# Performance work log

Measured on AMD Instinct MI355X. Metric: run time of the kernel, lower is better.

## Reference

```python
import jax, jax.numpy as jnp
import numpy as np

NUM_HEADS = 16
TEMPERATURE = 1.0
LN_EPS = 1e-5


def _layer_norm(x, g, b):
    m = x.mean(-1, keepdims=True)
    v = ((x - m) ** 2).mean(-1, keepdims=True)
    return (x - m) / jnp.sqrt(v + LN_EPS) * g + b


def _forward(input_ids, k, tok_emb, pos_emb, Wqkv, bqkv, Wo, bo, ln1g, ln1b, ln2g, ln2b,
             W1, b1, W2, b2, Wr, br, We1, be1, We2, be2, Wout, bout):
    B, S = input_ids.shape
    D = tok_emb.shape[1]
    L = Wqkv.shape[0]
    H = NUM_HEADS
    dh = D // H
    # embeddings: token + learned position
    x = tok_emb[input_ids] + pos_emb[:S][None, :, :]  # [B,S,D]

    # post-norm TransformerEncoder (PyTorch default), gelu FFN, no mask (attention_mask=None path)
    for i in range(L):
        qkv = jnp.einsum('bsd,ed->bse', x, Wqkv[i]) + bqkv[i]        # [B,S,3D]
        q, kk, v = jnp.split(qkv, 3, axis=-1)
        to_heads = lambda t: t.reshape(B, S, H, dh).transpose(0, 2, 1, 3)  # [B,H,S,dh]
        q, kk, v = to_heads(q), to_heads(kk), to_heads(v)
        scores = jnp.einsum('bhqd,bhkd->bhqk', q, kk) / np.float32(np.sqrt(dh))
        attn = jax.nn.softmax(scores, axis=-1)
        ctx = jnp.einsum('bhqk,bhkd->bhqd', attn, v).transpose(0, 2, 1, 3).reshape(B, S, D)
        attn_out = jnp.einsum('bsd,ed->bse', ctx, Wo[i]) + bo[i]
        x = _layer_norm(x + attn_out, ln1g[i], ln1b[i])
        ff = jnp.einsum('bsf,df->bsd',
                        jax.nn.gelu(jnp.einsum('bsd,fd->bsf', x, W1[i]) + b1[i], approximate=False),
                        W2[i]) + b2[i]
        x = _layer_norm(x + ff, ln2g[i], ln2b[i])

    # router: top-k over softmax(logits / T), renormalized top-k weights
    T = B * S
    h = x.reshape(T, D)
    rlogits = h @ Wr.T + br                         # [T,E]
    probs = jax.nn.softmax(rlogits / TEMPERATURE, axis=-1)
    w, idx = jax.lax.top_k(probs, k)                # [T,k]
    w = w / w.sum(-1, keepdims=True)

    # experts (GELU MLP), computed densely and combined with one-hot routing weights
    E = We1.shape[0]
    hid = jax.nn.gelu(jnp.einsum('td,efd->etf', h, We1) + be1[:, None, :], approximate=False)  # [E,T,F]
    eout = jnp.einsum('etf,edf->etd', hid, We2) + be2[:, None, :]                              # [E,T,D]
    comb = (jax.nn.one_hot(idx, E, dtype=h.dtype) * w[..., None]).sum(1)                       # [T,E]
    moe = jnp.einsum('etd,te->td', eout, comb)                                                 # [T,D]

    logits = moe @ Wout.T + bout
    return logits.reshape(B, S, -1)


def setup_inputs() -> dict:
    key = jax.random.key(0)
    ks = iter(jax.random.split(key, 32))
    B, S, D, L, V, E, F, K = 4, 512, 1024, 12, 32000, 8, 4096, 2
    p = lambda shape: jax.random.normal(next(ks), shape, dtype=jnp.float32) * 0.02
    return {
        'input_ids': jax.random.randint(next(ks), (B, S), 0, V, dtype=jnp.int32),
        'k': K,
        'tok_emb': p((V, D)), 'pos_emb': p((1024, D)),
        'Wqkv': p((L, 3 * D, D)), 'bqkv': jnp.zeros((L, 3 * D), jnp.float32),
        'Wo': p((L, D, D)), 'bo': jnp.zeros((L, D), jnp.float32),
        'ln1g': jnp.ones((L, D), jnp.float32), 'ln1b': jnp.zeros((L, D), jnp.float32),
        'ln2g': jnp.ones((L, D), jnp.float32), 'ln2b': jnp.zeros((L, D), jnp.float32),
        'W1': p((L, F, D)), 'b1': jnp.zeros((L, F), jnp.float32),
        'W2': p((L, D, F)), 'b2': jnp.zeros((L, D), jnp.float32),
        'Wr': p((E, D)), 'br': jnp.zeros((E,), jnp.float32),
        'We1': p((E, F, D)), 'be1': jnp.zeros((E, F), jnp.float32),
        'We2': p((E, D, F)), 'be2': jnp.zeros((E, D), jnp.float32),
        'Wout': p((V, D)), 'bout': jnp.zeros((V,), jnp.float32),
    }


def reference(input_ids, k, tok_emb, pos_emb, Wqkv, bqkv, Wo, bo, ln1g, ln1b, ln2g, ln2b,
              W1, b1, W2, b2, Wr, br, We1, be1, We2, be2, Wout, bout):
    return _forward(input_ids, k, tok_emb, pos_emb, Wqkv, bqkv, Wo, bo, ln1g, ln1b, ln2g, ln2b,
                    W1, b1, W2, b2, Wr, br, We1, be1, We2, be2, Wout, bout)
```

## Files before the change

### kernel.cpp

```cpp
#include <hip/hip_runtime.h>
#include <cstdint>
#include <cstddef>

#define DI __device__ __forceinline__

typedef __attribute__((ext_vector_type(8))) short short8;
typedef __attribute__((ext_vector_type(4))) float f32x4;
typedef unsigned short u16;

DI u16 f2bf(float f) {
  union { float f; unsigned u; } v; v.f = f;
  unsigned r = v.u + 0x7fffu + ((v.u >> 16) & 1u);
  return (u16)(r >> 16);
}
DI float bf2f(u16 h) {
  union { unsigned u; float f; } v; v.u = ((unsigned)h) << 16;
  return v.f;
}

DI void gload_lds16(const void* g, void* l) {
  __builtin_amdgcn_global_load_lds(
      (const __attribute__((address_space(1))) void*)g,
      (__attribute__((address_space(3))) void*)l, 16, 0, 0);
}

DI void atomAddF(float* p, float v) {
  __hip_atomic_fetch_add(p, v, __ATOMIC_RELAXED, __HIP_MEMORY_SCOPE_AGENT);
}

DI void split4(float4 v, uint2& hi, uint2& lo) {
  unsigned u0 = __float_as_uint(v.x), u1 = __float_as_uint(v.y);
  unsigned u2 = __float_as_uint(v.z), u3 = __float_as_uint(v.w);
  unsigned r0 = (u0 + 0x7fffu + ((u0 >> 16) & 1u)) & 0xffff0000u;
  unsigned r1 = (u1 + 0x7fffu + ((u1 >> 16) & 1u)) & 0xffff0000u;
  unsigned r2 = (u2 + 0x7fffu + ((u2 >> 16) & 1u)) & 0xffff0000u;
  unsigned r3 = (u3 + 0x7fffu + ((u3 >> 16) & 1u)) & 0xffff0000u;
  unsigned l0 = __float_as_uint(v.x - __uint_as_float(r0));
  unsigned l1 = __float_as_uint(v.y - __uint_as_float(r1));
  unsigned l2 = __float_as_uint(v.z - __uint_as_float(r2));
  unsigned l3 = __float_as_uint(v.w - __uint_as_float(r3));
  hi.x = __builtin_amdgcn_perm(r1, r0, 0x07060302u);
  hi.y = __builtin_amdgcn_perm(r3, r2, 0x07060302u);
  lo.x = __builtin_amdgcn_perm(l1, l0, 0x07060302u);
  lo.y = __builtin_amdgcn_perm(l3, l2, 0x07060302u);
}

template<int BM, int BN, int WGM, int WGN, int OUTMODE, bool GELU, int GATHER,
         bool BF32, int SPLITK, int TERMS>
__global__ __launch_bounds__(256)
void gemm_bt(const u16* __restrict__ A, int lda, long planeA, long offA_hi, long offA_lo,
             const void* __restrict__ Bv, int ldb, long planeB, long offB_hi, long offB_lo,
             void* __restrict__ Cv, int ldc, long planeC, long offC_hi, long offC_lo,
             int K, float alpha,
             const float* __restrict__ bias, long offBias,
             const float* __restrict__ wf,
             const int* __restrict__ glist,
             const int* __restrict__ gcnt,
             const int* __restrict__ gmap,
             const int* __restrict__ gaoff)
{
  constexpr int BK = 32;
  constexpr int WM = BM / WGM, WN = BN / WGN;
  constexpr int FM = WM / 16, FN = WN / 16;
  constexpr int A_INST = (BM * BK) / (256 * 8);
  constexpr int B_INST = (BN * BK) / (256 * 8);
  constexpr int BF_INST = (BN * BK) / (256 * 4);
  static_assert(A_INST * 2048 == BM * BK && B_INST * 2048 == BN * BK, "tile sizing");

  int bx = blockIdx.x, by = blockIdx.y;
  {
    const int gy = gridDim.y;
    const int nwg = gridDim.x * gy;
    const int id = bx * gy + by;
    const int q = nwg >> 3, r = nwg & 7;
    const int xcd = id & 7, pos = id >> 3;
    const int nid = ((xcd < r) ? xcd * (q + 1) : r * (q + 1) + (xcd - r) * q) + pos;
    bx = nid / gy; by = nid % gy;
  }

  int e = 0, sk = 0, zb = 0, zh = 0, cnte = 0, lsb = 0;
  if constexpr (GATHER != 0) {
    e = gmap[by];
    if (e < 0) return;
    cnte = gcnt[e];
    lsb = by * BM - gaoff[e];
    if constexpr (SPLITK > 1) sk = blockIdx.z;
  } else if constexpr (SPLITK > 1) {
    sk = blockIdx.z;
  } else {
    zb = blockIdx.z >> 4; zh = blockIdx.z & 15;
  }

  __shared__ __align__(16) u16 Ash[BM * BK];
  __shared__ __align__(16) u16 Asl[BM * BK];
  __shared__ __align__(16) u16 Bsh[BN * BK];
  __shared__ __align__(16) u16 Bsl[(TERMS == 3) ? BN * BK : 8];

  const int tid = threadIdx.x;
  const int lane = tid & 63, wid = tid >> 6;

  const u16* Ab = A + (size_t)zb * offA_hi + (size_t)zh * offA_lo
                    + (GATHER == 1 ? 0 : (size_t)(by * BM) * lda);
  const u16* Bb = (const u16*)Bv + (size_t)zb * offB_hi + (size_t)zh * offB_lo
                    + (size_t)(bx * BN) * ldb;
  const float* Bfb = (const float*)Bv + (size_t)e * offB_hi
                    + (size_t)(bx * BN) * ldb;

  int grow[A_INST];
  if constexpr (GATHER == 1) {
#pragma unroll
    for (int j = 0; j < A_INST; ++j) {
      int ee = (j * 256 + tid) * 8;
      int sl = lsb + (ee >> 5);
      grow[j] = (sl < cnte) ? (glist[e * 2048 + sl] >> 1) : 0;
    }
  }

  const int wm0 = (wid / WGN) * WM;
  const int wn0 = (wid % WGN) * WN;
  const int fr = lane & 15;
  const int kb = (lane >> 4) * 8;

  f32x4 acc[FM][FN] = {};

  const int Ksp = K / SPLITK;
  const int kbeg = sk * Ksp, kend = kbeg + Ksp;
  for (int k0 = kbeg; k0 < kend; k0 += BK) {
    __syncthreads();
#pragma unroll
    for (int j = 0; j < A_INST; ++j) {
      int ee = (j * 256 + tid) * 8;
      size_t gs = (GATHER == 1 ? (size_t)grow[j] : (size_t)(ee >> 5)) * lda + k0 + (ee & 31);
      gload_lds16(Ab + gs,          (char*)Ash + (size_t)ee * 2);
      gload_lds16(Ab + planeA + gs, (char*)Asl + (size_t)ee * 2);
    }
    if constexpr (BF32) {
#pragma unroll
      for (int j = 0; j < BF_INST; ++j) {
        int ee = (j * 256 + tid) * 4;
        float4 v = *(const float4*)(Bfb + (size_t)(ee >> 5) * ldb + k0 + (ee & 31));
        uint2 hi, lo;
        split4(v, hi, lo);
        *(uint2*)&Bsh[ee] = hi;
        if constexpr (TERMS == 3) *(uint2*)&Bsl[ee] = lo;
      }
    } else {
#pragma unroll
      for (int j = 0; j < B_INST; ++j) {
        int ee = (j * 256 + tid) * 8;
        size_t gs = (size_t)(ee >> 5) * ldb + k0 + (ee & 31);
        gload_lds16(Bb + gs, (char*)Bsh + (size_t)ee * 2);
        if constexpr (TERMS == 3)
          gload_lds16(Bb + planeB + gs, (char*)Bsl + (size_t)ee * 2);
      }
    }
    __syncthreads();

    short8 ah[FM], al_[FM], bh[FN], bl[FN];
#pragma unroll
    for (int mi = 0; mi < FM; ++mi) {
      int off = (wm0 + mi * 16 + fr) * BK + kb;
      ah[mi]  = *(const short8*)&Ash[off];
      al_[mi] = *(const short8*)&Asl[off];
    }
#pragma unroll
    for (int ni = 0; ni < FN; ++ni) {
      int off = (wn0 + ni * 16 + fr) * BK + kb;
      bh[ni] = *(const short8*)&Bsh[off];
      if constexpr (TERMS == 3) bl[ni] = *(const short8*)&Bsl[off];
    }
#pragma unroll
    for (int mi = 0; mi < FM; ++mi)
#pragma unroll
      for (int ni = 0; ni < FN; ++ni) {
        acc[mi][ni] = __builtin_amdgcn_mfma_f32_16x16x32_bf16(ah[mi],  bh[ni], acc[mi][ni], 0, 0, 0);
        if constexpr (TERMS == 3)
          acc[mi][ni] = __builtin_amdgcn_mfma_f32_16x16x32_bf16(ah[mi], bl[ni], acc[mi][ni], 0, 0, 0);
        acc[mi][ni] = __builtin_amdgcn_mfma_f32_16x16x32_bf16(al_[mi], bh[ni], acc[mi][ni], 0, 0, 0);
      }
  }
  __syncthreads();

  const size_t offC = (size_t)zb * offC_hi + (size_t)zh * offC_lo;
  const int row0 = by * BM + wm0 + (lane >> 4) * 4;
  const int col0 = bx * BN + wn0 + fr;
  const float* biasp = bias ? bias + (size_t)e * offBias : nullptr;
  const bool addBias = biasp && (SPLITK == 1 || sk == 0);

#pragma unroll
  for (int mi = 0; mi < FM; ++mi) {
#pragma unroll
    for (int ni = 0; ni < FN; ++ni) {
      const int col = col0 + ni * 16;
      const float bv = addBias ? biasp[col] : 0.f;
#pragma unroll
      for (int r = 0; r < 4; ++r) {
        const int row = row0 + mi * 16 + r;
        float v = acc[mi][ni][r] * alpha + bv;
        if constexpr (GELU) v = 0.5f * v * (1.f + erff(v * 0.70710678118f));
        if constexpr (OUTMODE == 4) {
          int sl = row - gaoff[e];
          if (sl < cnte) {
            int lv = glist[e * 2048 + sl];
            int tok = lv >> 1, rank = lv & 1;
            float* p = (float*)Cv + (size_t)rank * planeC + (size_t)tok * ldc + col;
            float out = wf[tok * 2 + rank] * v;
            if constexpr (SPLITK > 1) atomAddF(p, out); else *p = out;
          }
        } else {
          const size_t idx = offC + (size_t)row * ldc + col;
          if constexpr (OUTMODE == 1) {
            u16 h = f2bf(v);
            u16 l = f2bf(v - bf2f(h));
            ((u16*)Cv)[idx] = h;
            ((u16*)Cv)[idx + planeC] = l;
          } else if constexpr (OUTMODE == 3) {
            if constexpr (SPLITK > 1) atomAddF((float*)Cv + idx, v);
            else ((float*)Cv)[idx] += v;
          } else {
            ((float*)Cv)[idx] = v;
          }
        }
      }
    }
  }
}

__global__ __launch_bounds__(512)
void attn_scores(const u16* __restrict__ qkv, long planeQ,
                 u16* __restrict__ probs, long planeP)
{
  constexpr int BK = 32, S = 512;
  extern __shared__ __align__(16) char smem[];
  u16* Ash = (u16*)smem;
  u16* Asl = Ash + 128 * 32;
  u16* Bsh = Asl + 128 * 32;
  u16* Bsl = Bsh + 512 * 32;
  float* redM = (float*)(Bsl + 512 * 32);
  float* redS = redM + 512;

  const int tid = threadIdx.x, lane = tid & 63, wid = tid >> 6;
  const int bh = blockIdx.z, zb = bh >> 4, zh = bh & 15;
  const int qt = blockIdx.y;
  const u16* Ab = qkv + (size_t)zb * (512 * 3072) + (size_t)zh * 64
                      + (size_t)(qt * 128) * 3072;
  const u16* Bb = qkv + (size_t)zb * (512 * 3072) + (size_t)zh * 64 + 1024;

  const int wr = wid >> 2, wc = wid & 3;
  const int fr = lane & 15, kb = (lane >> 4) * 8, g = lane >> 4;

  f32x4 acc[4][8] = {};

  for (int k0 = 0; k0 < 64; k0 += BK) {
    __syncthreads();
    {
      int ee = tid * 8;
      size_t gs = (size_t)(ee >> 5) * 3072 + k0 + (ee & 31);
      gload_lds16(Ab + gs,          (char*)Ash + (size_t)ee * 2);
      gload_lds16(Ab + planeQ + gs, (char*)Asl + (size_t)ee * 2);
    }
#pragma unroll
    for (int j = 0; j < 4; ++j) {
      int ee = (j * 512 + tid) * 8;
      size_t gs = (size_t)(ee >> 5) * 3072 + k0 + (ee & 31);
      gload_lds16(Bb + gs,          (char*)Bsh + (size_t)ee * 2);
      gload_lds16(Bb + planeQ + gs, (char*)Bsl + (size_t)ee * 2);
    }
    __syncthreads();

    short8 ah[4], al_[4];
#pragma unroll
    for (int mi = 0; mi < 4; ++mi) {
      int off = (wr * 64 + mi * 16 + fr) * BK + kb;
      ah[mi]  = *(const short8*)&Ash[off];
      al_[mi] = *(const short8*)&Asl[off];
    }
#pragma unroll
    for (int ni = 0; ni < 8; ++ni) {
      int off = (wc * 128 + ni * 16 + fr) * BK + kb;
      short8 bhv = *(const short8*)&Bsh[off];
      short8 blv = *(const short8*)&Bsl[off];
#pragma unroll
      for (int mi = 0; mi < 4; ++mi) {
        acc[mi][ni] = __builtin_amdgcn_mfma_f32_16x16x32_bf16(ah[mi],  bhv, acc[mi][ni], 0, 0, 0);
        acc[mi][ni] = __builtin_amdgcn_mfma_f32_16x16x32_bf16(ah[mi],  blv, acc[mi][ni], 0, 0, 0);
        acc[mi][ni] = __builtin_amdgcn_mfma_f32_16x16x32_bf16(al_[mi], bhv, acc[mi][ni], 0, 0, 0);
      }
    }
  }

#pragma unroll
  for (int mi = 0; mi < 4; ++mi)
#pragma unroll
    for (int ni = 0; ni < 8; ++ni)
#pragma unroll
      for (int r = 0; r < 4; ++r) acc[mi][ni][r] *= 0.125f;

  float m[4][4];
#pragma unroll
  for (int mi = 0; mi < 4; ++mi)
#pragma unroll
    for (int r = 0; r < 4; ++r) {
      float v = acc[mi][0][r];
#pragma unroll
      for (int ni = 1; ni < 8; ++ni) v = fmaxf(v, acc[mi][ni][r]);
      v = fmaxf(v, __shfl_xor(v, 1));
      v = fmaxf(v, __shfl_xor(v, 2));
      v = fmaxf(v, __shfl_xor(v, 4));
      v = fmaxf(v, __shfl_xor(v, 8));
      m[mi][r] = v;
    }
  if (fr == 0) {
#pragma unroll
    for (int mi = 0; mi < 4; ++mi)
#pragma unroll
      for (int r = 0; r < 4; ++r)
        redM[wr * 256 + (g * 4 + mi * 16 + r) * 4 + wc] = m[mi][r];
  }
  __syncthreads();
#pragma unroll
  for (int mi = 0; mi < 4; ++mi)
#pragma unroll
    for (int r = 0; r < 4; ++r) {
      const float* p = &redM[wr * 256 + (g * 4 + mi * 16 + r) * 4];
      m[mi][r] = fmaxf(fmaxf(p[0], p[1]), fmaxf(p[2], p[3]));
    }

  float ssum[4][4];
#pragma unroll
  for (int mi = 0; mi < 4; ++mi)
#pragma unroll
    for (int r = 0; r < 4; ++r) {
      float ss = 0.f;
#pragma unroll
      for (int ni = 0; ni < 8; ++ni) {
        float p = __expf(acc[mi][ni][r] - m[mi][r]);
        acc[mi][ni][r] = p;
        ss += p;
      }
      ss += __shfl_xor(ss, 1);
      ss += __shfl_xor(ss, 2);
      ss += __shfl_xor(ss, 4);
      ss += __shfl_xor(ss, 8);
      ssum[mi][r] = ss;
    }
  if (fr == 0) {
#pragma unroll
    for (int mi = 0; mi < 4; ++mi)
#pragma unroll
      for (int r = 0; r < 4; ++r)
        redS[wr * 256 + (g * 4 + mi * 16 + r) * 4 + wc] = ssum[mi][r];
  }
  __syncthreads();

  const size_t base = (size_t)bh * S * S + (size_t)(qt * 128 + wr * 64) * S;
#pragma unroll
  for (int mi = 0; mi < 4; ++mi)
#pragma unroll
    for (int r = 0; r < 4; ++r) {
      const float* p = &redS[wr * 256 + (g * 4 + mi * 16 + r) * 4];
      const float inv = 1.f / (p[0] + p[1] + p[2] + p[3]);
      const size_t rowoff = base + (size_t)(g * 4 + mi * 16 + r) * S;
#pragma unroll
      for (int ni = 0; ni < 8; ++ni) {
        float pv = acc[mi][ni][r] * inv;
        u16 h = f2bf(pv);
        u16 l = f2bf(pv - bf2f(h));
        size_t idx = rowoff + wc * 128 + ni * 16 + fr;
        probs[idx] = h;
        probs[idx + planeP] = l;
      }
    }
}

__global__ __launch_bounds__(256)
void embed_kernel(const int* __restrict__ ids, const float* __restrict__ tok,
                  const float* __restrict__ pos, float* __restrict__ x,
                  u16* __restrict__ xs, long plane)
{
  const int t = blockIdx.x, c = threadIdx.x;
  const int id = ids[t], s = t & 511;
  float4 tv = ((const float4*)(tok + (size_t)id * 1024))[c];
  float4 pv = ((const float4*)(pos + (size_t)s * 1024))[c];
  float o[4] = {tv.x + pv.x, tv.y + pv.y, tv.z + pv.z, tv.w + pv.w};
  ((float4*)(x + (size_t)t * 1024))[c] = *(float4*)o;
  uint2 uh, ul;
  u16 h0 = f2bf(o[0]), h1 = f2bf(o[1]), h2 = f2bf(o[2]), h3 = f2bf(o[3]);
  uh.x = (unsigned)h0 | ((unsigned)h1 << 16);
  uh.y = (unsigned)h2 | ((unsigned)h3 << 16);
  ul.x = (unsigned)f2bf(o[0] - bf2f(h0)) | ((unsigned)f2bf(o[1] - bf2f(h1)) << 16);
  ul.y = (unsigned)f2bf(o[2] - bf2f(h2)) | ((unsigned)f2bf(o[3] - bf2f(h3)) << 16);
  const size_t idx = (size_t)t * 1024 + c * 4;
  *(uint2*)(xs + idx) = uh;
  *(uint2*)(xs + plane + idx) = ul;
}

__global__ __launch_bounds__(256)
void ln_kernel(float* __restrict__ x, const float* __restrict__ g,
               const float* __restrict__ b, u16* __restrict__ xs, long plane)
{
  const int row = blockIdx.x, t = threadIdx.x;
  float4 xv = ((const float4*)(x + (size_t)row * 1024))[t];
  float s = xv.x + xv.y + xv.z + xv.w;
  float q = xv.x * xv.x + xv.y * xv.y + xv.z * xv.z + xv.w * xv.w;
#pragma unroll
  for (int o = 32; o; o >>= 1) { s += __shfl_xor(s, o); q += __shfl_xor(q, o); }
  __shared__ float ss[4], qq[4];
  const int wid = t >> 6;
  if ((t & 63) == 0) { ss[wid] = s; qq[wid] = q; }
  __syncthreads();
  s = ss[0] + ss[1] + ss[2] + ss[3];
  q = qq[0] + qq[1] + qq[2] + qq[3];
  const float mean = s * (1.f / 1024.f);
  const float var = q * (1.f / 1024.f) - mean * mean;
  const float rstd = 1.f / sqrtf(var + 1e-5f);
  float4 gv = ((const float4*)g)[t];
  float4 bv = ((const float4*)b)[t];
  float o[4];
  o[0] = (xv.x - mean) * rstd * gv.x + bv.x;
  o[1] = (xv.y - mean) * rstd * gv.y + bv.y;
  o[2] = (xv.z - mean) * rstd * gv.z + bv.z;
  o[3] = (xv.w - mean) * rstd * gv.w + bv.w;
  ((float4*)(x + (size_t)row * 1024))[t] = *(float4*)o;
  uint2 uh, ul;
  u16 h0 = f2bf(o[0]), h1 = f2bf(o[1]), h2 = f2bf(o[2]), h3 = f2bf(o[3]);
  uh.x = (unsigned)h0 | ((unsigned)h1 << 16);
  uh.y = (unsigned)h2 | ((unsigned)h3 << 16);
  ul.x = (unsigned)f2bf(o[0] - bf2f(h0)) | ((unsigned)f2bf(o[1] - bf2f(h1)) << 16);
  ul.y = (unsigned)f2bf(o[2] - bf2f(h2)) | ((unsigned)f2bf(o[3] - bf2f(h3)) << 16);
  const size_t idx = (size_t)row * 1024 + t * 4;
  *(uint2*)(xs + idx) = uh;
  *(uint2*)(xs + plane + idx) = ul;
}

__global__ __launch_bounds__(256)
void vtrans_kernel(const u16* __restrict__ qkv, u16* __restrict__ vT,
                   long planeQ, long planeV)
{
  __shared__ u16 tile[64][68];
  const u16* src = qkv + (size_t)blockIdx.z * planeQ;
  u16* dst = vT + (size_t)blockIdx.z * planeV;
  const int s0 = blockIdx.x << 6;
  const int bh = blockIdx.y, b = bh >> 4, h = bh & 15;
  const int t = threadIdx.x;
#pragma unroll
  for (int j = 0; j < 16; ++j) {
    int idx = j * 256 + t;
    int sl = idx >> 6, d = idx & 63;
    tile[sl][d] = src[(size_t)(b * 512 + s0 + sl) * 3072 + 2048 + h * 64 + d];
  }
  __syncthreads();
#pragma unroll
  for (int j = 0; j < 16; ++j) {
    int idx = j * 256 + t;
    int d = idx >> 6, sl = idx & 63;
    dst[(size_t)bh * (64 * 512) + (size_t)d * 512 + s0 + sl] = tile[sl][d];
  }
}

__global__ __launch_bounds__(256)
void router_kernel(const float* __restrict__ x, const float* __restrict__ Wr,
                   const float* __restrict__ br, int2* __restrict__ er,
                   float2* __restrict__ wf)
{
  const int lane = threadIdx.x & 63, wid = threadIdx.x >> 6;
  const int t = blockIdx.x * 4 + wid;
  const float* xr = x + (size_t)t * 1024;
  float xv[16];
#pragma unroll
  for (int j = 0; j < 16; ++j) xv[j] = xr[j * 64 + lane];
  float p[8];
#pragma unroll
  for (int e = 0; e < 8; ++e) {
    const float* wr = Wr + (size_t)e * 1024;
    float s = 0.f;
#pragma unroll
    for (int j = 0; j < 16; ++j) s += xv[j] * wr[j * 64 + lane];
#pragma unroll
    for (int o = 32; o; o >>= 1) s += __shfl_xor(s, o);
    p[e] = s + br[e];
  }
  float m = p[0];
#pragma unroll
  for (int e = 1; e < 8; ++e) m = fmaxf(m, p[e]);
#pragma unroll
  for (int e = 0; e < 8; ++e) p[e] = __expf(p[e] - m);
  int i1 = -1; float v1 = -1.f;
#pragma unroll
  for (int e = 0; e < 8; ++e) if (p[e] > v1) { v1 = p[e]; i1 = e; }
  int i2 = -1; float v2 = -1.f;
#pragma unroll
  for (int e = 0; e < 8; ++e) if (e != i1 && p[e] > v2) { v2 = p[e]; i2 = e; }
  const float inv = 1.f / (v1 + v2);
  if (lane == 0) {
    er[t] = make_int2(i1, i2);
    wf[t] = make_float2(v1 * inv, v2 * inv);
  }
}

__global__ __launch_bounds__(256)
void build_lists(const int2* __restrict__ er, int* __restrict__ cnt,
                 int* __restrict__ list)
{
  const int t = blockIdx.x * 256 + threadIdx.x;
  int2 e = er[t];
  int s0 = atomicAdd(&cnt[e.x], 1); list[e.x * 2048 + s0] = t * 2;
  int s1 = atomicAdd(&cnt[e.y], 1); list[e.y * 2048 + s1] = t * 2 + 1;
}

__global__ void finalize_lists(const int* __restrict__ cnt, int* __restrict__ aoff,
                               int* __restrict__ block2e, int nb)
{
  if (threadIdx.x != 0 || blockIdx.x != 0) return;
  for (int b = 0; b < nb; ++b) block2e[b] = -1;
  int off = 0;
  for (int e = 0; e < 8; ++e) {
    aoff[e] = off;
    int pe = ((cnt[e] + 127) >> 7) << 7;
    for (int b = off >> 7; b < (off + pe) >> 7; ++b) block2e[b] = e;
    off += pe;
  }
  aoff[8] = off;
}

__global__ __launch_bounds__(256)
void combine_split(const float* __restrict__ o0, const float* __restrict__ o1,
                   u16* __restrict__ dh, long plane)
{
  const long i = ((long)blockIdx.x * 256 + threadIdx.x) * 8;
  float4 a0 = ((const float4*)o0)[i / 4];
  float4 a1 = ((const float4*)o0)[i / 4 + 1];
  float4 b0 = ((const float4*)o1)[i / 4];
  float4 b1 = ((const float4*)o1)[i / 4 + 1];
  float v[8] = {a0.x + b0.x, a0.y + b0.y, a0.z + b0.z, a0.w + b0.w,
                a1.x + b1.x, a1.y + b1.y, a1.z + b1.z, a1.w + b1.w};
  u16 h[8], l[8];
#pragma unroll
  for (int j = 0; j < 8; ++j) {
    h[j] = f2bf(v[j]);
    l[j] = f2bf(v[j] - bf2f(h[j]));
  }
  uint4 uh, ul;
  uh.x = (unsigned)h[0] | ((unsigned)h[1] << 16); ul.x = (unsigned)l[0] | ((unsigned)l[1] << 16);
  uh.y = (unsigned)h[2] | ((unsigned)h[3] << 16); ul.y = (unsigned)l[2] | ((unsigned)l[3] << 16);
  uh.z = (unsigned)h[4] | ((unsigned)h[5] << 16); ul.z = (unsigned)l[4] | ((unsigned)l[5] << 16);
  uh.w = (unsigned)h[6] | ((unsigned)h[7] << 16); ul.w = (unsigned)l[6] | ((unsigned)l[7] << 16);
  ((uint4*)dh)[i / 8] = uh;
  ((uint4*)(dh + plane))[i / 8] = ul;
}


extern "C" void kernel_launch(void* const* d_in, const int* in_sizes, int n_in,
                              void* d_out, int out_size, void* d_ws, size_t ws_size,
                              hipStream_t stream)
{
  (void)in_sizes; (void)n_in; (void)out_size;
  const int*   ids  = (const int*)d_in[0];
  const float* tok  = (const float*)d_in[2];
  const float* pos  = (const float*)d_in[3];
  const float* Wqkv = (const float*)d_in[4];
  const float* bqkv = (const float*)d_in[5];
  const float* Wo   = (const float*)d_in[6];
  const float* bo   = (const float*)d_in[7];
  const float* ln1g = (const float*)d_in[8];
  const float* ln1b = (const float*)d_in[9];
  const float* ln2g = (const float*)d_in[10];
  const float* ln2b = (const float*)d_in[11];
  const float* W1   = (const float*)d_in[12];
  const float* b1   = (const float*)d_in[13];
  const float* W2   = (const float*)d_in[14];
  const float* b2   = (const float*)d_in[15];
  const float* Wr   = (const float*)d_in[16];
  const float* br   = (const float*)d_in[17];
  const float* We1  = (const float*)d_in[18];
  const float* be1  = (const float*)d_in[19];
  const float* We2  = (const float*)d_in[20];
  const float* be2  = (const float*)d_in[21];
  const float* Wout = (const float*)d_in[22];
  const float* bout = (const float*)d_in[23];

  constexpr int T = 2048, D = 1024, S = 512, Bb = 4, H = 16, dh = 64, F = 4096,
                L = 12, E = 8, V = 32000;
  constexpr int NB = (2 * T + E * 127) / 128 + 1;

  constexpr long PX  = (long)T * D;
  constexpr long PQ  = (long)T * 3 * D;
  constexpr long PFE = (long)(NB * 128) * F;
  constexpr long PV  = (long)Bb * H * dh * S;
  constexpr long PSC = (long)Bb * H * S * S;

  char* w = (char*)d_ws;
  size_t o = 0;
  auto alloc = [&](size_t bytes) -> void* {
    void* p = w + o; o = (o + bytes + 255) & ~(size_t)255; return p;
  };
  float* x    = (float*)alloc((size_t)T * D * 4);
  u16* xs   = (u16*)alloc((size_t)2 * PX * 2);
  u16* moes = (u16*)alloc((size_t)2 * PX * 2);
  u16* qkvs = (u16*)alloc((size_t)2 * PQ * 2);
  u16* ctxs = (u16*)alloc((size_t)2 * PX * 2);
  size_t bigsz = (size_t)2 * ((PSC > PFE ? PSC : PFE)) * 2;
  u16* big  = (u16*)alloc(bigsz);
  u16* ffs  = big;
  u16* scs  = big;
  u16* vTs  = (u16*)alloc((size_t)2 * PV * 2);
  float* outr = (float*)alloc((size_t)2 * PX * 4);
  int2*   er  = (int2*)alloc((size_t)T * 8);
  float2* wf  = (float2*)alloc((size_t)T * 8);
  int*    cnt = (int*)alloc((size_t)E * 4);
  int*    list= (int*)alloc((size_t)E * T * 4);
  int*    aoff= (int*)alloc((size_t)(E + 1) * 4);
  int*    b2e = (int*)alloc((size_t)NB * 4);
  if (o > ws_size) return;

  embed_kernel<<<T, 256, 0, stream>>>(ids, tok, pos, x, xs, PX);

  constexpr size_t ATTN_LDS = (4096 + 4096 + 16384 + 16384) * 2 + 2 * 512 * 4;

  for (int l = 0; l < L; ++l) {
    gemm_bt<128,128,2,2,1,false,0,true,1,3><<<dim3(3 * D / 128, T / 128, 1), 256, 0, stream>>>(
        xs, D, PX, 0, 0, Wqkv + (size_t)l * 3 * D * D, D, 0, 0, 0,
        qkvs, 3 * D, PQ, 0, 0, D, 1.f, bqkv + (size_t)l * 3 * D, 0,
        nullptr, nullptr, nullptr, nullptr, nullptr);
    vtrans_kernel<<<dim3(S / 64, Bb * H, 2), 256, 0, stream>>>(qkvs, vTs, PQ, PV);
    attn_scores<<<dim3(1, S / 128, Bb * H), 512, ATTN_LDS, stream>>>(qkvs, PQ, scs, PSC);
    gemm_bt<64,64,2,2,1,false,0,false,1,3><<<dim3(1, S / 64, Bb * H), 256, 0, stream>>>(
        scs, S, PSC, (long)H * S * S, (long)S * S,
        vTs, S, PV,  (long)H * dh * S, (long)dh * S,
        ctxs, D, PX, (long)S * D, (long)dh,
        S, 1.f, nullptr, 0, nullptr, nullptr, nullptr, nullptr, nullptr);
    gemm_bt<128,128,2,2,3,false,0,true,2,3><<<dim3(D / 128, T / 128, 2), 256, 0, stream>>>(
        ctxs, D, PX, 0, 0, Wo + (size_t)l * D * D, D, 0, 0, 0,
        x, D, 0, 0, 0, D, 1.f, bo + (size_t)l * D, 0,
        nullptr, nullptr, nullptr, nullptr, nullptr);
    ln_kernel<<<T, 256, 0, stream>>>(x, ln1g + (size_t)l * D, ln1b + (size_t)l * D, xs, PX);
    gemm_bt<128,128,2,2,1,true,0,true,1,3><<<dim3(F / 128, T / 128, 1), 256, 0, stream>>>(
        xs, D, PX, 0, 0, W1 + (size_t)l * F * D, D, 0, 0, 0,
        ffs, F, (long)T * F, 0, 0, D, 1.f, b1 + (size_t)l * F, 0,
        nullptr, nullptr, nullptr, nullptr, nullptr);
    gemm_bt<128,128,2,2,3,false,0,true,4,3><<<dim3(D / 128, T / 128, 4), 256, 0, stream>>>(
        ffs, F, (long)T * F, 0, 0, W2 + (size_t)l * D * F, F, 0, 0, 0,
        x, D, 0, 0, 0, F, 1.f, b2 + (size_t)l * D, 0,
        nullptr, nullptr, nullptr, nullptr, nullptr);
    ln_kernel<<<T, 256, 0, stream>>>(x, ln2g + (size_t)l * D, ln2b + (size_t)l * D, xs, PX);
  }

  router_kernel<<<T / 4, 256, 0, stream>>>(x, Wr, br, er, wf);
  hipMemsetAsync(cnt, 0, E * 4, stream);
  build_lists<<<T / 256, 256, 0, stream>>>(er, cnt, list);
  finalize_lists<<<1, 64, 0, stream>>>(cnt, aoff, b2e, NB);
  hipMemsetAsync(outr, 0, (size_t)2 * PX * 4, stream);

  gemm_bt<128,128,2,2,1,true,1,true,1,2><<<dim3(F / 128, NB, 1), 256, 0, stream>>>(
      xs, D, PX, 0, 0, We1, D, 0, (long)F * D, 0,
      ffs, F, PFE, 0, 0, D, 1.f, be1, F,
      nullptr, list, cnt, b2e, aoff);
  gemm_bt<128,128,2,2,4,false,2,true,2,2><<<dim3(D / 128, NB, 2), 256, 0, stream>>>(
      ffs, F, PFE, 0, 0, We2, F, 0, (long)D * F, 0,
      outr, D, PX, 0, 0, F, 1.f, be2, D,
      (const float*)wf, list, cnt, b2e, aoff);

  combine_split<<<(PX / 2048), 256, 0, stream>>>(outr, outr + PX, moes, PX);

  gemm_bt<128,128,2,2,0,false,0,true,1,2><<<dim3(V / 128, T / 128, 1), 256, 0, stream>>>(
      moes, D, PX, 0, 0, Wout, D, 0, 0, 0,
      (float*)d_out, V, 0, 0, 0,
      D, 1.f, bout, 0, nullptr, nullptr, nullptr, nullptr, nullptr);
}
```

Measured before the change: 4.619 ms.

## Fuse attention softmax with P·V and pre-convert output projection weights to bf16

```diff
diff --git a/kernel.cpp b/kernel.cpp
--- a/kernel.cpp
+++ b/kernel.cpp
@@ -227,8 +227,9 @@
 }
 
 __global__ __launch_bounds__(512)
-void attn_scores(const u16* __restrict__ qkv, long planeQ,
-                 u16* __restrict__ probs, long planeP)
+void attn_fused(const u16* __restrict__ qkv, long planeQ,
+                const u16* __restrict__ vT, long planeV,
+                u16* __restrict__ ctxs, long planeC)
 {
   constexpr int BK = 32, S = 512;
   extern __shared__ __align__(16) char smem[];
@@ -238,6 +239,10 @@
   u16* Bsl = Bsh + 512 * 32;
   float* redM = (float*)(Bsl + 512 * 32);
   float* redS = redM + 512;
+  u16* Ph = (u16*)smem;
+  u16* Pl = Ph + 128 * 32;
+  u16* Vh = Pl + 128 * 32;
+  u16* Vl = Vh + 64 * 32;
 
   const int tid = threadIdx.x, lane = tid & 63, wid = tid >> 6;
   const int bh = blockIdx.z, zb = bh >> 4, zh = bh & 15;
@@ -245,6 +250,7 @@
   const u16* Ab = qkv + (size_t)zb * (512 * 3072) + (size_t)zh * 64
                       + (size_t)(qt * 128) * 3072;
   const u16* Bb = qkv + (size_t)zb * (512 * 3072) + (size_t)zh * 64 + 1024;
+  const u16* vt = vT + (size_t)bh * (64 * 512);
 
   const int wr = wid >> 2, wc = wid & 3;
   const int fr = lane & 15, kb = (lane >> 4) * 8, g = lane >> 4;
@@ -353,23 +359,70 @@
   }
   __syncthreads();
 
-  const size_t base = (size_t)bh * S * S + (size_t)(qt * 128 + wr * 64) * S;
 #pragma unroll
   for (int mi = 0; mi < 4; ++mi)
 #pragma unroll
     for (int r = 0; r < 4; ++r) {
       const float* p = &redS[wr * 256 + (g * 4 + mi * 16 + r) * 4];
       const float inv = 1.f / (p[0] + p[1] + p[2] + p[3]);
-      const size_t rowoff = base + (size_t)(g * 4 + mi * 16 + r) * S;
-#pragma unroll
-      for (int ni = 0; ni < 8; ++ni) {
-        float pv = acc[mi][ni][r] * inv;
-        u16 h = f2bf(pv);
-        u16 l = f2bf(pv - bf2f(h));
-        size_t idx = rowoff + wc * 128 + ni * 16 + fr;
-        probs[idx] = h;
-        probs[idx + planeP] = l;
-      }
+#pragma unroll
+      for (int ni = 0; ni < 8; ++ni) acc[mi][ni][r] *= inv;
+    }
+
+  f32x4 c[4] = {};
+#pragma unroll
+  for (int ks = 0; ks < 16; ++ks) {
+    const int k0 = ks * 32;
+    __syncthreads();
+    if (wc == (ks >> 2)) {
+      const int ni0 = (ks & 3) * 2;
+#pragma unroll
+      for (int mi = 0; mi < 4; ++mi)
+#pragma unroll
+        for (int dni = 0; dni < 2; ++dni)
+#pragma unroll
+          for (int r = 0; r < 4; ++r) {
+            float v = acc[mi][ni0 + dni][r];
+            u16 h = f2bf(v);
+            u16 lo = f2bf(v - bf2f(h));
+            int row = wr * 64 + mi * 16 + g * 4 + r;
+            int koff = dni * 16 + fr;
+            Ph[row * 32 + koff] = h;
+            Pl[row * 32 + koff] = lo;
+          }
+    }
+    {
+      int ee = (tid & 255) * 8;
+      size_t gs = (size_t)(ee >> 5) * 512 + k0 + (ee & 31);
+      if (tid < 256) gload_lds16(vt + gs,          (char*)Vh + (size_t)ee * 2);
+      else           gload_lds16(vt + planeV + gs, (char*)Vl + (size_t)ee * 2);
+    }
+    __syncthreads();
+
+    short8 pah = *(const short8*)&Ph[(wid * 16 + fr) * 32 + kb];
+    short8 pal = *(const short8*)&Pl[(wid * 16 + fr) * 32 + kb];
+#pragma unroll
+    for (int ni = 0; ni < 4; ++ni) {
+      short8 vbh = *(const short8*)&Vh[(ni * 16 + fr) * 32 + kb];
+      short8 vbl = *(const short8*)&Vl[(ni * 16 + fr) * 32 + kb];
+      c[ni] = __builtin_amdgcn_mfma_f32_16x16x32_bf16(pah, vbh, c[ni], 0, 0, 0);
+      c[ni] = __builtin_amdgcn_mfma_f32_16x16x32_bf16(pah, vbl, c[ni], 0, 0, 0);
+      c[ni] = __builtin_amdgcn_mfma_f32_16x16x32_bf16(pal, vbh, c[ni], 0, 0, 0);
+    }
+  }
+
+#pragma unroll
+  for (int ni = 0; ni < 4; ++ni)
+#pragma unroll
+    for (int r = 0; r < 4; ++r) {
+      int row = qt * 128 + wid * 16 + g * 4 + r;
+      int d = ni * 16 + fr;
+      size_t idx = ((size_t)zb * 512 + row) * 1024 + zh * 64 + d;
+      float v = c[ni][r];
+      u16 h = f2bf(v);
+      u16 lo = f2bf(v - bf2f(h));
+      ctxs[idx] = h;
+      ctxs[idx + planeC] = lo;
     }
 }
 
@@ -549,6 +602,20 @@
   ((uint4*)(dh + plane))[i / 8] = ul;
 }
 
+__global__ __launch_bounds__(256)
+void trunc_bf16(const float* __restrict__ s, u16* __restrict__ d)
+{
+  const long i = ((long)blockIdx.x * 256 + threadIdx.x) * 8;
+  float4 a = ((const float4*)s)[i / 4];
+  float4 b = ((const float4*)s)[i / 4 + 1];
+  uint4 u;
+  u.x = (unsigned)f2bf(a.x) | ((unsigned)f2bf(a.y) << 16);
+  u.y = (unsigned)f2bf(a.z) | ((unsigned)f2bf(a.w) << 16);
+  u.z = (unsigned)f2bf(b.x) | ((unsigned)f2bf(b.y) << 16);
+  u.w = (unsigned)f2bf(b.z) | ((unsigned)f2bf(b.w) << 16);
+  ((uint4*)d)[i / 8] = u;
+}
+
 
 extern "C" void kernel_launch(void* const* d_in, const int* in_sizes, int n_in,
                               void* d_out, int out_size, void* d_ws, size_t ws_size,
@@ -587,7 +654,6 @@
   constexpr long PQ  = (long)T * 3 * D;
   constexpr long PFE = (long)(NB * 128) * F;
   constexpr long PV  = (long)Bb * H * dh * S;
-  constexpr long PSC = (long)Bb * H * S * S;
 
   char* w = (char*)d_ws;
   size_t o = 0;
@@ -599,11 +665,9 @@
   u16* moes = (u16*)alloc((size_t)2 * PX * 2);
   u16* qkvs = (u16*)alloc((size_t)2 * PQ * 2);
   u16* ctxs = (u16*)alloc((size_t)2 * PX * 2);
-  size_t bigsz = (size_t)2 * ((PSC > PFE ? PSC : PFE)) * 2;
-  u16* big  = (u16*)alloc(bigsz);
-  u16* ffs  = big;
-  u16* scs  = big;
+  u16* ffs  = (u16*)alloc((size_t)2 * PFE * 2);
   u16* vTs  = (u16*)alloc((size_t)2 * PV * 2);
+  u16* woutb = (u16*)alloc((size_t)V * D * 2);
   float* outr = (float*)alloc((size_t)2 * PX * 4);
   int2*   er  = (int2*)alloc((size_t)T * 8);
   float2* wf  = (float2*)alloc((size_t)T * 8);
@@ -614,6 +678,7 @@
   if (o > ws_size) return;
 
   embed_kernel<<<T, 256, 0, stream>>>(ids, tok, pos, x, xs, PX);
+  trunc_bf16<<<(V * D) / 2048, 256, 0, stream>>>(Wout, woutb);
 
   constexpr size_t ATTN_LDS = (4096 + 4096 + 16384 + 16384) * 2 + 2 * 512 * 4;
 
@@ -623,12 +688,8 @@
         qkvs, 3 * D, PQ, 0, 0, D, 1.f, bqkv + (size_t)l * 3 * D, 0,
         nullptr, nullptr, nullptr, nullptr, nullptr);
     vtrans_kernel<<<dim3(S / 64, Bb * H, 2), 256, 0, stream>>>(qkvs, vTs, PQ, PV);
-    attn_scores<<<dim3(1, S / 128, Bb * H), 512, ATTN_LDS, stream>>>(qkvs, PQ, scs, PSC);
-    gemm_bt<64,64,2,2,1,false,0,false,1,3><<<dim3(1, S / 64, Bb * H), 256, 0, stream>>>(
-        scs, S, PSC, (long)H * S * S, (long)S * S,
-        vTs, S, PV,  (long)H * dh * S, (long)dh * S,
-        ctxs, D, PX, (long)S * D, (long)dh,
-        S, 1.f, nullptr, 0, nullptr, nullptr, nullptr, nullptr, nullptr);
+    attn_fused<<<dim3(1, S / 128, Bb * H), 512, ATTN_LDS, stream>>>(
+        qkvs, PQ, vTs, PV, ctxs, PX);
     gemm_bt<128,128,2,2,3,false,0,true,2,3><<<dim3(D / 128, T / 128, 2), 256, 0, stream>>>(
         ctxs, D, PX, 0, 0, Wo + (size_t)l * D * D, D, 0, 0, 0,
         x, D, 0, 0, 0, D, 1.f, bo + (size_t)l * D, 0,
@@ -662,8 +723,8 @@
 
   combine_split<<<(PX / 2048), 256, 0, stream>>>(outr, outr + PX, moes, PX);
 
-  gemm_bt<128,128,2,2,0,false,0,true,1,2><<<dim3(V / 128, T / 128, 1), 256, 0, stream>>>(
-      moes, D, PX, 0, 0, Wout, D, 0, 0, 0,
+  gemm_bt<128,128,2,2,0,false,0,false,1,2><<<dim3(V / 128, T / 128, 1), 256, 0, stream>>>(
+      moes, D, PX, 0, 0, woutb, D, 0, 0, 0,
       (float*)d_out, V, 0, 0, 0,
       D, 1.f, bout, 0, nullptr, nullptr, nullptr, nullptr, nullptr);
 }
```

Measured after the change: 4.450 ms. -3.7%, faster.
